# Optimization experiments

Hardware: AMD Instinct MI355X
Metric: run time of the kernel (lower is better)

The kernel has to match this reference:

```python
import jax, jax.numpy as jnp
import numpy as np

D_MODEL = 1024
D_STATE = 128
D_CONV = 4
EXPAND = 2
HEADDIM = 64
D_INNER = EXPAND * D_MODEL            # 2048
NHEADS = D_INNER // HEADDIM           # 32
D_IN_PROJ = 2 * D_INNER + 2 * D_STATE + NHEADS  # z, xBC, dt
CONV_DIM = D_INNER + 2 * D_STATE      # depthwise-conv channels


def setup_inputs() -> dict:
    key = jax.random.key(0)
    ks = jax.random.split(key, 8)
    B, L = 2, 2048
    s = lambda k, shape, sc=0.02: jax.random.normal(k, shape, jnp.float32) * sc
    return dict(
        x=jax.random.normal(ks[0], (B, L, D_MODEL), jnp.float32),
        norm1_w=jnp.ones((D_MODEL,), jnp.float32),
        in_proj_w=s(ks[1], (D_IN_PROJ, D_MODEL)),
        conv_w=s(ks[2], (CONV_DIM, D_CONV), 0.2),
        conv_b=jnp.zeros((CONV_DIM,), jnp.float32),
        dt_bias=jnp.log(jnp.expm1(jax.random.uniform(ks[3], (NHEADS,), jnp.float32, 0.001, 0.1))),
        A_log=jnp.log(jax.random.uniform(ks[4], (NHEADS,), jnp.float32, 1.0, 16.0)),
        D=jnp.ones((NHEADS,), jnp.float32),
        mnorm_w=jnp.ones((D_INNER,), jnp.float32),
        out_proj_w=s(ks[5], (D_MODEL, D_INNER)),
        norm2_w=jnp.ones((D_MODEL,), jnp.float32),
        mlp_w1=s(ks[6], (4 * D_MODEL, D_MODEL)),
        mlp_b1=jnp.zeros((4 * D_MODEL,), jnp.float32),
        mlp_w2=s(ks[7], (D_MODEL, 4 * D_MODEL)),
        mlp_b2=jnp.zeros((D_MODEL,), jnp.float32),
    )


def _block_norm(x, w, eps=1e-6):
    # Faithful to source: rms = sqrt(||x||_2^2 + eps) (their .mean(-1) is over a size-1 dim)
    return w * x / jnp.sqrt(jnp.sum(x * x, axis=-1, keepdims=True) + eps)


def _mamba2(x, in_proj_w, conv_w, conv_b, dt_bias, A_log, D, mnorm_w, out_proj_w):
    b, l, _ = x.shape
    zxbcdt = x @ in_proj_w.T                                   # (b,l,D_IN_PROJ)
    z, xBC, dt_raw = jnp.split(zxbcdt, [D_INNER, D_INNER + CONV_DIM], axis=-1)
    # causal depthwise conv1d + silu over (x,B,C)
    pad = jnp.pad(xBC, ((0, 0), (D_CONV - 1, 0), (0, 0)))
    conv = sum(pad[:, k:k + l, :] * conv_w[None, None, :, k] for k in range(D_CONV)) + conv_b
    xBC = jax.nn.silu(conv)
    xh, Bm, Cm = jnp.split(xBC, [D_INNER, D_INNER + D_STATE], axis=-1)
    xh = xh.reshape(b, l, NHEADS, HEADDIM)
    dt = jax.nn.softplus(dt_raw + dt_bias)                     # (b,l,h)
    A = -jnp.exp(A_log)                                        # (h,) scalar-A per head

    def step(hs, inp):
        x_t, dt_t, B_t, C_t = inp                              # (b,h,p),(b,h),(b,n),(b,n)
        dA = jnp.exp(dt_t * A)[:, :, None, None]               # (b,h,1,1)
        hs = hs * dA + (dt_t[:, :, None] * x_t)[..., None] * B_t[:, None, None, :]
        y_t = jnp.einsum('bhpn,bn->bhp', hs, C_t)
        return hs, y_t

    hs0 = jnp.zeros((b, NHEADS, HEADDIM, D_STATE), x.dtype)
    _, ys = jax.lax.scan(step, hs0, (xh.transpose(1, 0, 2, 3), dt.transpose(1, 0, 2),
                                     Bm.transpose(1, 0, 2), Cm.transpose(1, 0, 2)))
    y = ys.transpose(1, 0, 2, 3) + D[None, None, :, None] * xh  # D skip
    y = y.reshape(b, l, D_INNER)
    y = y * jax.nn.silu(z)                                      # gated RMSNorm (mamba2 default)
    y = y / jnp.sqrt(jnp.mean(y * y, axis=-1, keepdims=True) + 1e-5) * mnorm_w
    return y @ out_proj_w.T


def reference(x, norm1_w, in_proj_w, conv_w, conv_b, dt_bias, A_log, D, mnorm_w,
              out_proj_w, norm2_w, mlp_w1, mlp_b1, mlp_w2, mlp_b2):
    x = x + _mamba2(_block_norm(x, norm1_w), in_proj_w, conv_w, conv_b,
                    dt_bias, A_log, D, mnorm_w, out_proj_w)
    h = _block_norm(x, norm2_w)
    h = jax.nn.gelu(h @ mlp_w1.T + mlp_b1, approximate=False) @ mlp_w2.T + mlp_b2
    return x + h
```

## Files before the change

### kernel.cpp

```cpp
#include <hip/hip_runtime.h>
#include <hip/hip_bf16.h>
#include <cstdint>

#define L_SEQ   2048
#define BATCH   2
#define ROWS    (BATCH*L_SEQ)
#define DMODEL  1024
#define DINNER  2048
#define DSTATE  128
#define NHEADS  32
#define DIN_PROJ 4384
#define DIN_PAD  4480
#define CONVDIM  2304
#define DMLP    4096
#define CHUNK   64
#define NCHUNK  (L_SEQ/CHUNK)

typedef __attribute__((ext_vector_type(4))) float f32x4;
typedef __attribute__((ext_vector_type(8))) short bf16x8;
typedef __attribute__((ext_vector_type(4))) short bf16x4;
typedef __attribute__((ext_vector_type(2))) short bf16x2;

static __device__ __forceinline__ short f2bf(float f) {
  union { float f; unsigned int i; } v; v.f = f;
  unsigned int r = v.i + 0x7fffu + ((v.i >> 16) & 1u);
  return (short)(r >> 16);
}
static __device__ __forceinline__ float bf2f(short s) {
  union { unsigned int i; float f; } v; v.i = ((unsigned int)(unsigned short)s) << 16;
  return v.f;
}

static __device__ __forceinline__ void gl2lds16(const void* g, void* l) {
  __builtin_amdgcn_global_load_lds((const __attribute__((address_space(1))) void*)g,
                                   (__attribute__((address_space(3))) void*)l, 16, 0, 0);
}

__global__ __launch_bounds__(256) void cvt_kernel(const float* __restrict__ src, short* __restrict__ dst,
                                                  long rows_src, int kshift)
{
  long i = (((long)blockIdx.x) * 256 + threadIdx.x) * 4;
  long r = i >> kshift;
  bf16x4 o;
  if (r < rows_src) {
    f32x4 v = *(const f32x4*)&src[i];
    o[0] = f2bf(v[0]); o[1] = f2bf(v[1]); o[2] = f2bf(v[2]); o[3] = f2bf(v[3]);
  } else {
    o[0] = 0; o[1] = 0; o[2] = 0; o[3] = 0;
  }
  *(bf16x4*)&dst[i] = o;
}

__global__ __launch_bounds__(256) void rmsnorm_l2_kernel(const float* __restrict__ in,
                                                         const float* __restrict__ w,
                                                         short* __restrict__ out)
{
  int row = blockIdx.x, tid = threadIdx.x;
  const float* xr = in + (long)row * DMODEL;
  f32x4 v = *(const f32x4*)&xr[tid * 4];
  float s = v[0]*v[0] + v[1]*v[1] + v[2]*v[2] + v[3]*v[3];
  for (int o = 32; o; o >>= 1) s += __shfl_down(s, o);
  __shared__ float red[4];
  if ((tid & 63) == 0) red[tid >> 6] = s;
  __syncthreads();
  float sc = rsqrtf(red[0] + red[1] + red[2] + red[3] + 1e-6f);
  f32x4 wv = *(const f32x4*)&w[tid * 4];
  bf16x4 o;
  #pragma unroll
  for (int j = 0; j < 4; j++) o[j] = f2bf(v[j] * sc * wv[j]);
  *(bf16x4*)&out[(long)row * DMODEL + tid * 4] = o;
}

template<int EPI, int STG>
__global__ __launch_bounds__(256)
void gemm_bt_kernel(const short* __restrict__ A, const short* __restrict__ W,
                    const float* __restrict__ bias, const float* __restrict__ resid,
                    void* __restrict__ out, int N, int K)
{
  __shared__ short As[STG][128*64];
  __shared__ short Ws[STG][128*64];
  const int tid = threadIdx.x;
  const int lane = tid & 63, wid = tid >> 6;
  const int wm = wid >> 1, wn = wid & 1;
  const long arow0 = (long)blockIdx.x * 128;
  const long wrow0 = (long)blockIdx.y * 128;
  const int srow = tid >> 3;
  const int sslot = (tid & 7) ^ (srow & 7);
  const int sdst = (tid >> 3) * 64 + (tid & 7) * 8;

  f32x4 acc[4][4];
  #pragma unroll
  for (int m = 0; m < 4; m++)
    #pragma unroll
    for (int n = 0; n < 4; n++)
      #pragma unroll
      for (int j = 0; j < 4; j++) acc[m][n][j] = 0.f;

  auto stage = [&](int buf, int kt) {
    #pragma unroll
    for (int i = 0; i < 4; i++)
      gl2lds16(A + (arow0 + i*32 + srow) * (long)K + kt + sslot*8, &As[buf][i*2048 + sdst]);
    #pragma unroll
    for (int i = 0; i < 4; i++)
      gl2lds16(W + (wrow0 + i*32 + srow) * (long)K + kt + sslot*8, &Ws[buf][i*2048 + sdst]);
  };

  const int nt = K >> 6;
  #pragma unroll
  for (int s = 0; s < STG - 1; s++) stage(s, s << 6);

  const int swz = (lane & 7) << 3;
  for (int t = 0; t < nt; t++) {
    if (t + STG - 1 < nt) {
      stage((t + STG - 1) & (STG - 1), (t + STG - 1) << 6);
      if (STG == 4) asm volatile("s_waitcnt vmcnt(24)" ::: "memory");
      else          asm volatile("s_waitcnt vmcnt(8)"  ::: "memory");
    } else if (STG == 4 && t + 2 < nt) {
      asm volatile("s_waitcnt vmcnt(16)" ::: "memory");
    } else if (STG == 4 && t + 1 < nt) {
      asm volatile("s_waitcnt vmcnt(8)" ::: "memory");
    } else {
      asm volatile("s_waitcnt vmcnt(0)" ::: "memory");
    }
    __builtin_amdgcn_s_barrier();
    __builtin_amdgcn_sched_barrier(0);
    const int cur = t & (STG - 1);
    #pragma unroll
    for (int kk = 0; kk < 64; kk += 32) {
      bf16x8 a[4], b[4];
      const int ko = kk + (lane >> 4) * 8;
      #pragma unroll
      for (int m = 0; m < 4; m++) {
        int row = wm*64 + m*16 + (lane & 15);
        a[m] = *(const bf16x8*)&As[cur][(row*64 + ko) ^ swz];
      }
      #pragma unroll
      for (int n = 0; n < 4; n++) {
        int row = wn*64 + n*16 + (lane & 15);
        b[n] = *(const bf16x8*)&Ws[cur][(row*64 + ko) ^ swz];
      }
      #pragma unroll
      for (int m = 0; m < 4; m++)
        #pragma unroll
        for (int n = 0; n < 4; n++)
          acc[m][n] = __builtin_amdgcn_mfma_f32_16x16x32_bf16(a[m], b[n], acc[m][n], 0, 0, 0);
    }
    asm volatile("s_waitcnt lgkmcnt(0)" ::: "memory");
    __builtin_amdgcn_sched_barrier(0);
    __builtin_amdgcn_s_barrier();
  }

  const int colf = lane & 15, rowf = (lane >> 4) * 4;
  #pragma unroll
  for (int m = 0; m < 4; m++)
    #pragma unroll
    for (int n = 0; n < 4; n++) {
      long col = wrow0 + wn*64 + n*16 + colf;
      #pragma unroll
      for (int j = 0; j < 4; j++) {
        long row = arow0 + wm*64 + m*16 + rowf + j;
        long idx = row * (long)N + col;
        float v = acc[m][n][j];
        if (EPI == 0) {
          ((short*)out)[idx] = f2bf(v);
        } else if (EPI == 1) {
          ((float*)out)[idx] = v + resid[idx];
        } else if (EPI == 2) {
          float t = v + bias[col];
          float ge = 0.5f * t * (1.f + erff(t * 0.70710678118654752f));
          ((short*)out)[idx] = f2bf(ge);
        } else {
          ((float*)out)[idx] = v + bias[col] + resid[idx];
        }
      }
    }
}

__global__ __launch_bounds__(256) void conv_dt_kernel(
    const short* __restrict__ zx, const float* __restrict__ cw, const float* __restrict__ cb,
    const float* __restrict__ dt_bias,
    short* __restrict__ xh, short* __restrict__ Bo, short* __restrict__ Co, float* __restrict__ dto)
{
  const int r0 = blockIdx.x * 8;
  const int tid = threadIdx.x;
  const bool interior = (r0 & (L_SEQ - 1)) != 0;

  auto conv8 = [&](int c0, auto&& emit) {
    const long col = DINNER + c0;
    f32x4 w[8]; float cbv[8];
    #pragma unroll
    for (int j = 0; j < 8; j++) { w[j] = *(const f32x4*)&cw[(c0 + j) * 4]; cbv[j] = cb[c0 + j]; }
    bf16x8 win[11];
    #pragma unroll
    for (int j = 0; j < 3; j++) {
      bf16x8 z;
      #pragma unroll
      for (int q = 0; q < 8; q++) z[q] = 0;
      win[j] = interior ? *(const bf16x8*)&zx[(long)(r0 - 3 + j) * DIN_PAD + col] : z;
    }
    #pragma unroll
    for (int j = 3; j < 11; j++)
      win[j] = *(const bf16x8*)&zx[(long)(r0 - 3 + j) * DIN_PAD + col];
    #pragma unroll
    for (int i = 0; i < 8; i++) {
      float a[8];
      #pragma unroll
      for (int j = 0; j < 8; j++) a[j] = cbv[j];
      #pragma unroll
      for (int k = 0; k < 4; k++)
        #pragma unroll
        for (int j = 0; j < 8; j++) a[j] = fmaf(bf2f(win[i + k][j]), w[j][k], a[j]);
      bf16x8 o;
      #pragma unroll
      for (int j = 0; j < 8; j++) { float s = a[j] / (1.f + __expf(-a[j])); o[j] = f2bf(s); }
      emit(i, o);
    }
  };

  {
    int c0 = tid * 8;
    conv8(c0, [&](int i, bf16x8 o) {
      *(bf16x8*)&xh[(long)(r0 + i) * DINNER + c0] = o;
    });
  }
  if (tid < 32) {
    int c0 = 2048 + tid * 8;
    conv8(c0, [&](int i, bf16x8 o) {
      if (c0 < 2048 + DSTATE) *(bf16x8*)&Bo[(long)(r0 + i) * DSTATE + (c0 - 2048)] = o;
      else                    *(bf16x8*)&Co[(long)(r0 + i) * DSTATE + (c0 - 2048 - DSTATE)] = o;
    });
  } else if (tid < 36) {
    int h0 = (tid - 32) * 8;
    float db[8];
    #pragma unroll
    for (int j = 0; j < 8; j++) db[j] = dt_bias[h0 + j];
    #pragma unroll
    for (int i = 0; i < 8; i++) {
      bf16x8 v = *(const bf16x8*)&zx[(long)(r0 + i) * DIN_PAD + (DINNER + CONVDIM) + h0];
      f32x4 o0, o1;
      #pragma unroll
      for (int j = 0; j < 8; j++) {
        float t = bf2f(v[j]) + db[j];
        float sp = (t > 20.f) ? t : log1pf(__expf(t));
        if (j < 4) o0[j] = sp; else o1[j - 4] = sp;
      }
      *(f32x4*)&dto[(long)(r0 + i) * NHEADS + h0] = o0;
      *(f32x4*)&dto[(long)(r0 + i) * NHEADS + h0 + 4] = o1;
    }
  }
}


__global__ __launch_bounds__(256) void ssd_states_kernel(
    const short* __restrict__ xh, const short* __restrict__ Bm,
    const float* __restrict__ dtb, const float* __restrict__ A_log,
    float* __restrict__ CS, short* __restrict__ SC)
{
  int bid = blockIdx.x;
  int c = bid & 31, h = (bid >> 5) & 31, b = bid >> 10;
  long r0 = (long)b * L_SEQ + c * CHUNK;
  __shared__ short XT[64*72];
  __shared__ short BwT[128*72];
  __shared__ float ws[64];
  int tid = threadIdx.x;

  if (tid < 64) {
    float dtv = dtb[(r0 + tid)*NHEADS + h];
    float A = -__expf(A_log[h]);
    float v = dtv * A;
    #pragma unroll
    for (int o = 1; o < 64; o <<= 1) { float u = __shfl_up(v, o); if (tid >= o) v += u; }
    CS[(long)bid * 64 + tid] = v;
    float cs63 = __shfl(v, 63);
    ws[tid] = __expf(cs63 - v) * dtv;
  }
  #pragma unroll
  for (int i = 0; i < 2; i++) {
    int e = tid + i*256, tau = e & 63, p0 = (e >> 6) * 8;
    bf16x8 v = *(const bf16x8*)&xh[(r0 + tau)*DINNER + h*64 + p0];
    #pragma unroll
    for (int j = 0; j < 8; j++) XT[(p0 + j)*72 + tau] = v[j];
  }
  __syncthreads();
  #pragma unroll
  for (int i = 0; i < 4; i++) {
    int e = tid + i*256, tau = e & 63, n0 = (e >> 6) * 8;
    float w = ws[tau];
    bf16x8 v = *(const bf16x8*)&Bm[(r0 + tau)*DSTATE + n0];
    #pragma unroll
    for (int j = 0; j < 8; j++) BwT[(n0 + j)*72 + tau] = f2bf(bf2f(v[j]) * w);
  }
  __syncthreads();

  int lane = tid & 63, w = tid >> 6;
  f32x4 acc[8];
  #pragma unroll
  for (int nt = 0; nt < 8; nt++) { acc[nt][0]=0.f; acc[nt][1]=0.f; acc[nt][2]=0.f; acc[nt][3]=0.f; }
  #pragma unroll
  for (int kk = 0; kk < 64; kk += 32) {
    int ko = kk + (lane >> 4) * 8;
    bf16x8 a = *(const bf16x8*)&XT[(w*16 + (lane & 15))*72 + ko];
    #pragma unroll
    for (int nt = 0; nt < 8; nt++) {
      bf16x8 bfr = *(const bf16x8*)&BwT[(nt*16 + (lane & 15))*72 + ko];
      acc[nt] = __builtin_amdgcn_mfma_f32_16x16x32_bf16(a, bfr, acc[nt], 0, 0, 0);
    }
  }
  int colf = lane & 15, rowf = (lane >> 4) * 4;
  long sbase = (long)bid * 8192;
  #pragma unroll
  for (int nt = 0; nt < 8; nt++)
    #pragma unroll
    for (int j = 0; j < 4; j++)
      SC[sbase + (w*16 + rowf + j)*128 + nt*16 + colf] = f2bf(acc[nt][j]);
}

__global__ __launch_bounds__(256) void ssd_prefix_kernel(
    const short* __restrict__ SC, const float* __restrict__ CS, short* __restrict__ HP)
{
  int bid = blockIdx.x;
  int q = bid & 3, bh = bid >> 2;
  int tid = threadIdx.x;
  int p = q*16 + (tid >> 4);
  int n0 = (tid & 15) * 8;
  long base = (long)bh * NCHUNK * 8192 + (long)p*128 + n0;
  float H[8];
  #pragma unroll
  for (int j = 0; j < 8; j++) H[j] = 0.f;
  for (int c = 0; c < NCHUNK; c++) {
    long idx = base + (long)c * 8192;
    bf16x8 sc = *(const bf16x8*)&SC[idx];
    bf16x8 hv;
    #pragma unroll
    for (int j = 0; j < 8; j++) hv[j] = f2bf(H[j]);
    *(bf16x8*)&HP[idx] = hv;
    float r = __expf(CS[((long)bh * NCHUNK + c)*64 + 63]);
    #pragma unroll
    for (int j = 0; j < 8; j++) H[j] = H[j]*r + bf2f(sc[j]);
  }
}

__global__ __launch_bounds__(256) void ssd_out_kernel(
    const short* __restrict__ xh, const short* __restrict__ Bm, const short* __restrict__ Cm,
    const float* __restrict__ dtb, const float* __restrict__ CS,
    const short* __restrict__ HP, const float* __restrict__ Dvec,
    short* __restrict__ y)
{
  int bid = blockIdx.x;
  int c = bid & 31, h = (bid >> 5) & 31, b = bid >> 10;
  long r0 = (long)b * L_SEQ + c * CHUNK;
  __shared__ short Csh[64*136];
  __shared__ short Bsh[64*136];
  __shared__ short Ms[64*72];
  __shared__ short XT[64*72];
  __shared__ float csd[64], dts[64];
  int tid = threadIdx.x;

  if (tid < 64) {
    csd[tid] = CS[(long)bid*64 + tid];
    dts[tid] = dtb[(r0 + tid)*NHEADS + h];
  }
  #pragma unroll
  for (int i = 0; i < 4; i++) {
    int e = tid + i*256, tau = e >> 4, n0 = (e & 15) * 8;
    *(bf16x8*)&Bsh[tau*136 + n0] = *(const bf16x8*)&Bm[(r0 + tau)*DSTATE + n0];
    *(bf16x8*)&Csh[tau*136 + n0] = *(const bf16x8*)&Cm[(r0 + tau)*DSTATE + n0];
  }
  #pragma unroll
  for (int i = 0; i < 2; i++) {
    int e = tid + i*256, tau = e & 63, p0 = (e >> 6) * 8;
    bf16x8 v = *(const bf16x8*)&xh[(r0 + tau)*DINNER + h*64 + p0];
    #pragma unroll
    for (int j = 0; j < 8; j++) XT[(p0 + j)*72 + tau] = v[j];
  }
  __syncthreads();

  int lane = tid & 63, w = tid >> 6;
  int colf = lane & 15, rowf = (lane >> 4) * 4;

  f32x4 g[4];
  #pragma unroll
  for (int tt = 0; tt < 4; tt++) { g[tt][0]=0.f; g[tt][1]=0.f; g[tt][2]=0.f; g[tt][3]=0.f; }
  #pragma unroll
  for (int kk = 0; kk < 128; kk += 32) {
    int ko = kk + (lane >> 4) * 8;
    bf16x8 a = *(const bf16x8*)&Csh[(w*16 + (lane & 15))*136 + ko];
    #pragma unroll
    for (int tt = 0; tt < 4; tt++) {
      bf16x8 bfr = *(const bf16x8*)&Bsh[(tt*16 + (lane & 15))*136 + ko];
      g[tt] = __builtin_amdgcn_mfma_f32_16x16x32_bf16(a, bfr, g[tt], 0, 0, 0);
    }
  }
  #pragma unroll
  for (int tt = 0; tt < 4; tt++)
    #pragma unroll
    for (int j = 0; j < 4; j++) {
      int trow = w*16 + rowf + j;
      int tcol = tt*16 + colf;
      float m = (tcol <= trow) ? __expf(csd[trow] - csd[tcol]) * dts[tcol] * g[tt][j] : 0.f;
      Ms[trow*72 + tcol] = f2bf(m);
    }
  __syncthreads();

  f32x4 yv[4], yi[4];
  #pragma unroll
  for (int pt = 0; pt < 4; pt++) {
    yv[pt][0]=0.f; yv[pt][1]=0.f; yv[pt][2]=0.f; yv[pt][3]=0.f;
    yi[pt][0]=0.f; yi[pt][1]=0.f; yi[pt][2]=0.f; yi[pt][3]=0.f;
  }
  #pragma unroll
  for (int kk = 0; kk < 64; kk += 32) {
    int ko = kk + (lane >> 4) * 8;
    bf16x8 a = *(const bf16x8*)&Ms[(w*16 + (lane & 15))*72 + ko];
    #pragma unroll
    for (int pt = 0; pt < 4; pt++) {
      bf16x8 bfr = *(const bf16x8*)&XT[(pt*16 + (lane & 15))*72 + ko];
      yv[pt] = __builtin_amdgcn_mfma_f32_16x16x32_bf16(a, bfr, yv[pt], 0, 0, 0);
    }
  }
  long hpb = (long)bid * 8192;
  #pragma unroll
  for (int kk = 0; kk < 128; kk += 32) {
    int ko = kk + (lane >> 4) * 8;
    bf16x8 a = *(const bf16x8*)&Csh[(w*16 + (lane & 15))*136 + ko];
    #pragma unroll
    for (int pt = 0; pt < 4; pt++) {
      bf16x8 bfr = *(const bf16x8*)&HP[hpb + (long)(pt*16 + (lane & 15))*128 + ko];
      yi[pt] = __builtin_amdgcn_mfma_f32_16x16x32_bf16(a, bfr, yi[pt], 0, 0, 0);
    }
  }
  float Dh = Dvec[h];
  #pragma unroll
  for (int pt = 0; pt < 4; pt++)
    #pragma unroll
    for (int j = 0; j < 4; j++) {
      int trow = w*16 + rowf + j;
      int pcol = pt*16 + colf;
      float sc_ = __expf(csd[trow]);
      float xv = bf2f(XT[pcol*72 + trow]);
      y[(r0 + trow)*DINNER + h*64 + pcol] = f2bf(yv[pt][j] + sc_*yi[pt][j] + Dh*xv);
    }
}

__global__ __launch_bounds__(256) void gate_mnorm_kernel(
    const short* __restrict__ y, const short* __restrict__ zx, const float* __restrict__ mw,
    short* __restrict__ out)
{
  int row = blockIdx.x, tid = threadIdx.x;
  int c0 = tid * 8;
  bf16x8 yv = *(const bf16x8*)&y[(long)row*DINNER + c0];
  bf16x8 zv = *(const bf16x8*)&zx[(long)row*DIN_PAD + c0];
  float g[8]; float ssum = 0.f;
  #pragma unroll
  for (int j = 0; j < 8; j++) {
    float z = bf2f(zv[j]);
    float v = bf2f(yv[j]) * (z / (1.f + __expf(-z)));
    g[j] = v; ssum += v * v;
  }
  for (int o = 32; o; o >>= 1) ssum += __shfl_down(ssum, o);
  __shared__ float red[4];
  if ((tid & 63) == 0) red[tid >> 6] = ssum;
  __syncthreads();
  float tot = red[0] + red[1] + red[2] + red[3];
  float sc = rsqrtf(tot * (1.0f / DINNER) + 1e-5f);
  bf16x8 o;
  #pragma unroll
  for (int j = 0; j < 8; j++) o[j] = f2bf(g[j] * sc * mw[c0 + j]);
  *(bf16x8*)&out[(long)row*DINNER + c0] = o;
}

extern "C" void kernel_launch(void* const* d_in, const int* in_sizes, int n_in,
                              void* d_out, int out_size, void* d_ws, size_t ws_size,
                              hipStream_t stream)
{
  const float* x        = (const float*)d_in[0];
  const float* norm1_w  = (const float*)d_in[1];
  const float* in_proj  = (const float*)d_in[2];
  const float* conv_w   = (const float*)d_in[3];
  const float* conv_b   = (const float*)d_in[4];
  const float* dt_bias  = (const float*)d_in[5];
  const float* A_log    = (const float*)d_in[6];
  const float* Dvec     = (const float*)d_in[7];
  const float* mnorm_w  = (const float*)d_in[8];
  const float* out_proj = (const float*)d_in[9];
  const float* norm2_w  = (const float*)d_in[10];
  const float* mlp_w1   = (const float*)d_in[11];
  const float* mlp_b1   = (const float*)d_in[12];
  const float* mlp_w2   = (const float*)d_in[13];
  const float* mlp_b2   = (const float*)d_in[14];
  float* outp = (float*)d_out;

  uint8_t* wsp = (uint8_t*)d_ws;
  auto take = [&](size_t bytes) { void* p = wsp; wsp += (bytes + 255) & ~(size_t)255; return p; };
  short* W1B  = (short*)take((size_t)DIN_PAD * DMODEL * 2);
  short* W2B  = (short*)take((size_t)DMODEL * DINNER * 2);
  short* W3B  = (short*)take((size_t)DMLP * DMODEL * 2);
  short* W4B  = (short*)take((size_t)DMODEL * DMLP * 2);
  short* X1B  = (short*)take((size_t)ROWS * DMODEL * 2);
  short* ZX   = (short*)take((size_t)ROWS * DIN_PAD * 2);
  short* XH   = (short*)take((size_t)ROWS * DINNER * 2);
  short* BMb  = (short*)take((size_t)ROWS * DSTATE * 2);
  short* CMb  = (short*)take((size_t)ROWS * DSTATE * 2);
  float* DTb  = (float*)take((size_t)ROWS * NHEADS * 4);
  short* Yb   = (short*)take((size_t)ROWS * DINNER * 2);
  short* YGB  = (short*)take((size_t)ROWS * DINNER * 2);
  float* X2   = (float*)take((size_t)ROWS * DMODEL * 4);
  short* X2NB = (short*)take((size_t)ROWS * DMODEL * 2);
  short* H1B  = (short*)take((size_t)ROWS * DMLP * 2);

  short* SC = H1B;
  short* HP = YGB;
  float* CS = (float*)X2NB;

  cvt_kernel<<<4480, 256, 0, stream>>>(in_proj, W1B, DIN_PROJ, 10);
  cvt_kernel<<<2048, 256, 0, stream>>>(out_proj, W2B, DMODEL, 11);
  cvt_kernel<<<4096, 256, 0, stream>>>(mlp_w1, W3B, DMLP, 10);
  cvt_kernel<<<4096, 256, 0, stream>>>(mlp_w2, W4B, DMODEL, 12);

  rmsnorm_l2_kernel<<<ROWS, 256, 0, stream>>>(x, norm1_w, X1B);
  gemm_bt_kernel<0,2><<<dim3(ROWS/128, DIN_PAD/128), 256, 0, stream>>>(X1B, W1B, nullptr, nullptr, ZX, DIN_PAD, DMODEL);
  conv_dt_kernel<<<ROWS/8, 256, 0, stream>>>(ZX, conv_w, conv_b, dt_bias, XH, BMb, CMb, DTb);
  ssd_states_kernel<<<BATCH*NHEADS*NCHUNK, 256, 0, stream>>>(XH, BMb, DTb, A_log, CS, SC);
  ssd_prefix_kernel<<<BATCH*NHEADS*4, 256, 0, stream>>>(SC, CS, HP);
  ssd_out_kernel<<<BATCH*NHEADS*NCHUNK, 256, 0, stream>>>(XH, BMb, CMb, DTb, CS, HP, Dvec, Yb);
  gate_mnorm_kernel<<<ROWS, 256, 0, stream>>>(Yb, ZX, mnorm_w, YGB);
  gemm_bt_kernel<1,4><<<dim3(ROWS/128, DMODEL/128), 256, 0, stream>>>(YGB, W2B, nullptr, x, X2, DMODEL, DINNER);
  rmsnorm_l2_kernel<<<ROWS, 256, 0, stream>>>(X2, norm2_w, X2NB);
  gemm_bt_kernel<2,2><<<dim3(ROWS/128, DMLP/128), 256, 0, stream>>>(X2NB, W3B, mlp_b1, nullptr, H1B, DMLP, DMODEL);
  gemm_bt_kernel<3,4><<<dim3(ROWS/128, DMODEL/128), 256, 0, stream>>>(H1B, W4B, mlp_b2, X2, outp, DMODEL, DMLP);
}
```

Baseline: 355.3 us.

## Split-K the two N=1024 GEMMs with a separate reduction kernel

```diff
diff --git a/kernel.cpp b/kernel.cpp
--- a/kernel.cpp
+++ b/kernel.cpp
@@ -88,6 +88,9 @@
   const int sslot = (tid & 7) ^ (srow & 7);
   const int sdst = (tid >> 3) * 64 + (tid & 7) * 8;
 
+  const int Keff = K / gridDim.z;
+  const long kbase = (long)blockIdx.z * Keff;
+
   f32x4 acc[4][4];
   #pragma unroll
   for (int m = 0; m < 4; m++)
@@ -96,7 +99,7 @@
       #pragma unroll
       for (int j = 0; j < 4; j++) acc[m][n][j] = 0.f;
 
-  auto stage = [&](int buf, int kt) {
+  auto stage = [&](int buf, long kt) {
     #pragma unroll
     for (int i = 0; i < 4; i++)
       gl2lds16(A + (arow0 + i*32 + srow) * (long)K + kt + sslot*8, &As[buf][i*2048 + sdst]);
@@ -105,14 +108,14 @@
       gl2lds16(W + (wrow0 + i*32 + srow) * (long)K + kt + sslot*8, &Ws[buf][i*2048 + sdst]);
   };
 
-  const int nt = K >> 6;
-  #pragma unroll
-  for (int s = 0; s < STG - 1; s++) stage(s, s << 6);
+  const int nt = Keff >> 6;
+  #pragma unroll
+  for (int s = 0; s < STG - 1; s++) stage(s, kbase + (s << 6));
 
   const int swz = (lane & 7) << 3;
   for (int t = 0; t < nt; t++) {
     if (t + STG - 1 < nt) {
-      stage((t + STG - 1) & (STG - 1), (t + STG - 1) << 6);
+      stage((t + STG - 1) & (STG - 1), kbase + ((long)(t + STG - 1) << 6));
       if (STG == 4) asm volatile("s_waitcnt vmcnt(24)" ::: "memory");
       else          asm volatile("s_waitcnt vmcnt(8)"  ::: "memory");
     } else if (STG == 4 && t + 2 < nt) {
@@ -151,6 +154,7 @@
   }
 
   const int colf = lane & 15, rowf = (lane >> 4) * 4;
+  const long psliceoff = (long)blockIdx.z * ((long)gridDim.x * 128) * N;
   #pragma unroll
   for (int m = 0; m < 4; m++)
     #pragma unroll
@@ -163,17 +167,36 @@
         float v = acc[m][n][j];
         if (EPI == 0) {
           ((short*)out)[idx] = f2bf(v);
-        } else if (EPI == 1) {
-          ((float*)out)[idx] = v + resid[idx];
         } else if (EPI == 2) {
           float t = v + bias[col];
           float ge = 0.5f * t * (1.f + erff(t * 0.70710678118654752f));
           ((short*)out)[idx] = f2bf(ge);
         } else {
-          ((float*)out)[idx] = v + bias[col] + resid[idx];
+          ((float*)out)[psliceoff + idx] = v;
         }
       }
     }
+}
+
+template<bool BIAS>
+__global__ __launch_bounds__(256) void reduce_split2_kernel(
+    const float* __restrict__ part, const float* __restrict__ resid,
+    const float* __restrict__ bias, float* __restrict__ out)
+{
+  long i = ((long)blockIdx.x * 256 + threadIdx.x) * 4;
+  f32x4 p0 = *(const f32x4*)&part[i];
+  f32x4 p1 = *(const f32x4*)&part[i + (long)ROWS * DMODEL];
+  f32x4 r  = *(const f32x4*)&resid[i];
+  f32x4 o;
+  if (BIAS) {
+    f32x4 bv = *(const f32x4*)&bias[(int)(i & (DMODEL - 1))];
+    #pragma unroll
+    for (int j = 0; j < 4; j++) o[j] = p0[j] + p1[j] + r[j] + bv[j];
+  } else {
+    #pragma unroll
+    for (int j = 0; j < 4; j++) o[j] = p0[j] + p1[j] + r[j];
+  }
+  *(f32x4*)&out[i] = o;
 }
 
 __global__ __launch_bounds__(256) void conv_dt_kernel(
@@ -511,6 +534,7 @@
   short* SC = H1B;
   short* HP = YGB;
   float* CS = (float*)X2NB;
+  float* PART = (float*)ZX;
 
   cvt_kernel<<<4480, 256, 0, stream>>>(in_proj, W1B, DIN_PROJ, 10);
   cvt_kernel<<<2048, 256, 0, stream>>>(out_proj, W2B, DMODEL, 11);
@@ -524,8 +548,10 @@
   ssd_prefix_kernel<<<BATCH*NHEADS*4, 256, 0, stream>>>(SC, CS, HP);
   ssd_out_kernel<<<BATCH*NHEADS*NCHUNK, 256, 0, stream>>>(XH, BMb, CMb, DTb, CS, HP, Dvec, Yb);
   gate_mnorm_kernel<<<ROWS, 256, 0, stream>>>(Yb, ZX, mnorm_w, YGB);
-  gemm_bt_kernel<1,4><<<dim3(ROWS/128, DMODEL/128), 256, 0, stream>>>(YGB, W2B, nullptr, x, X2, DMODEL, DINNER);
+  gemm_bt_kernel<4,2><<<dim3(ROWS/128, DMODEL/128, 2), 256, 0, stream>>>(YGB, W2B, nullptr, nullptr, PART, DMODEL, DINNER);
+  reduce_split2_kernel<false><<<ROWS*DMODEL/1024, 256, 0, stream>>>(PART, x, nullptr, X2);
   rmsnorm_l2_kernel<<<ROWS, 256, 0, stream>>>(X2, norm2_w, X2NB);
   gemm_bt_kernel<2,2><<<dim3(ROWS/128, DMLP/128), 256, 0, stream>>>(X2NB, W3B, mlp_b1, nullptr, H1B, DMLP, DMODEL);
-  gemm_bt_kernel<3,4><<<dim3(ROWS/128, DMODEL/128), 256, 0, stream>>>(H1B, W4B, mlp_b2, X2, outp, DMODEL, DMLP);
-}
+  gemm_bt_kernel<4,2><<<dim3(ROWS/128, DMODEL/128, 2), 256, 0, stream>>>(H1B, W4B, nullptr, nullptr, PART, DMODEL, DMLP);
+  reduce_split2_kernel<true><<<ROWS*DMODEL/1024, 256, 0, stream>>>(PART, X2, mlp_b2, outp);
+}
```

Result: faster. 337.6 us (-5.0%).

## Add 256x256 GEMM kernel with split-K for out_proj and MLP GEMMs

Applied to the files above, without the earlier changes.

```diff
diff --git a/kernel.cpp b/kernel.cpp
--- a/kernel.cpp
+++ b/kernel.cpp
@@ -96,7 +96,7 @@
       #pragma unroll
       for (int j = 0; j < 4; j++) acc[m][n][j] = 0.f;
 
-  auto stage = [&](int buf, int kt) {
+  auto stage = [&](int buf, long kt) {
     #pragma unroll
     for (int i = 0; i < 4; i++)
       gl2lds16(A + (arow0 + i*32 + srow) * (long)K + kt + sslot*8, &As[buf][i*2048 + sdst]);
@@ -112,13 +112,8 @@
   const int swz = (lane & 7) << 3;
   for (int t = 0; t < nt; t++) {
     if (t + STG - 1 < nt) {
-      stage((t + STG - 1) & (STG - 1), (t + STG - 1) << 6);
-      if (STG == 4) asm volatile("s_waitcnt vmcnt(24)" ::: "memory");
-      else          asm volatile("s_waitcnt vmcnt(8)"  ::: "memory");
-    } else if (STG == 4 && t + 2 < nt) {
-      asm volatile("s_waitcnt vmcnt(16)" ::: "memory");
-    } else if (STG == 4 && t + 1 < nt) {
-      asm volatile("s_waitcnt vmcnt(8)" ::: "memory");
+      stage((t + STG - 1) & (STG - 1), (long)(t + STG - 1) << 6);
+      asm volatile("s_waitcnt vmcnt(8)"  ::: "memory");
     } else {
       asm volatile("s_waitcnt vmcnt(0)" ::: "memory");
     }
@@ -160,20 +155,151 @@
       for (int j = 0; j < 4; j++) {
         long row = arow0 + wm*64 + m*16 + rowf + j;
         long idx = row * (long)N + col;
+        ((short*)out)[idx] = f2bf(acc[m][n][j]);
+      }
+    }
+}
+
+template<int EPI>
+__global__ __launch_bounds__(512)
+void gemm256_kernel(const short* __restrict__ A, const short* __restrict__ W,
+                    const float* __restrict__ bias, void* __restrict__ out, int N, int K)
+{
+  __shared__ short As[2][2][8192];
+  __shared__ short Bs[2][2][8192];
+  const int tid = threadIdx.x;
+  const int lane = tid & 63, wid = tid >> 6;
+  const int wm = wid >> 2, wn = wid & 3;
+  const long arow0 = (long)blockIdx.x * 256;
+  const long wrow0 = (long)blockIdx.y * 256;
+  const int Kslice = K / gridDim.z;
+  const long kbase = (long)blockIdx.z * Kslice;
+  const int ntiles = Kslice >> 6;
+
+  const int sr0 = tid >> 2, sr1 = sr0 + 128;
+  const int ss  = tid & 3;
+  const int scb0 = ss ^ ((sr0 >> 1) & 3);
+  const int scb1 = ss ^ ((sr1 >> 1) & 3);
+  const int sdst0 = tid * 8, sdst1 = tid * 8 + 4096;
+
+  auto stageA = [&](int tau, int kh) {
+    long colb = kbase + (long)tau * 64 + kh * 32;
+    gl2lds16(A + (arow0 + sr0) * (long)K + colb + scb0 * 8, &As[tau & 1][kh][sdst0]);
+    gl2lds16(A + (arow0 + sr1) * (long)K + colb + scb1 * 8, &As[tau & 1][kh][sdst1]);
+  };
+  auto stageB = [&](int tau, int kh) {
+    long colb = kbase + (long)tau * 64 + kh * 32;
+    gl2lds16(W + (wrow0 + sr0) * (long)K + colb + scb0 * 8, &Bs[tau & 1][kh][sdst0]);
+    gl2lds16(W + (wrow0 + sr1) * (long)K + colb + scb1 * 8, &Bs[tau & 1][kh][sdst1]);
+  };
+
+  f32x4 acc[8][4];
+  #pragma unroll
+  for (int m = 0; m < 8; m++)
+    #pragma unroll
+    for (int n = 0; n < 4; n++)
+      #pragma unroll
+      for (int j = 0; j < 4; j++) acc[m][n][j] = 0.f;
+
+  const int li = lane & 15;
+  const int rcb = (((lane >> 4) ^ ((li >> 1) & 3))) * 8;
+
+  stageA(0,0); stageB(0,0); stageA(0,1); stageB(0,1); stageA(1,0); stageB(1,0);
+  asm volatile("s_waitcnt vmcnt(8)" ::: "memory");
+  __builtin_amdgcn_s_barrier();
+
+  bf16x8 a[8];
+  auto phase = [&](int g, int kh, int nh) {
+    const int buf = g & 1;
+    if (nh == 0) {
+      #pragma unroll
+      for (int m = 0; m < 8; m++)
+        a[m] = *(const bf16x8*)&As[buf][kh][(wm*128 + m*16 + li)*32 + rcb];
+    }
+    bf16x8 b0 = *(const bf16x8*)&Bs[buf][kh][(wn*64 + (nh*2    )*16 + li)*32 + rcb];
+    bf16x8 b1 = *(const bf16x8*)&Bs[buf][kh][(wn*64 + (nh*2 + 1)*16 + li)*32 + rcb];
+    if (kh == 0) {
+      if (g + 1 < ntiles) { if (nh == 0) stageA(g+1, 1); else stageB(g+1, 1); }
+    } else {
+      if (g + 2 < ntiles) { if (nh == 0) stageA(g+2, 0); else stageB(g+2, 0); }
+    }
+    __builtin_amdgcn_s_barrier();
+    asm volatile("s_waitcnt lgkmcnt(0)" ::: "memory");
+    __builtin_amdgcn_sched_barrier(0);
+    __builtin_amdgcn_s_setprio(1);
+    #pragma unroll
+    for (int m = 0; m < 8; m++) {
+      acc[m][nh*2    ] = __builtin_amdgcn_mfma_f32_16x16x32_bf16(a[m], b0, acc[m][nh*2    ], 0, 0, 0);
+      acc[m][nh*2 + 1] = __builtin_amdgcn_mfma_f32_16x16x32_bf16(a[m], b1, acc[m][nh*2 + 1], 0, 0, 0);
+    }
+    __builtin_amdgcn_s_setprio(0);
+    if (kh == 0 && nh == 1) {
+      if (g < ntiles - 1) asm volatile("s_waitcnt vmcnt(8)" ::: "memory");
+      else                asm volatile("s_waitcnt vmcnt(0)" ::: "memory");
+    } else if (kh == 1 && nh == 1 && g < ntiles - 1) {
+      if (g < ntiles - 2) asm volatile("s_waitcnt vmcnt(8)" ::: "memory");
+      else                asm volatile("s_waitcnt vmcnt(4)" ::: "memory");
+    }
+    __builtin_amdgcn_s_barrier();
+  };
+
+  for (int g = 0; g < ntiles; ++g) {
+    phase(g, 0, 0); phase(g, 0, 1); phase(g, 1, 0); phase(g, 1, 1);
+  }
+
+  const int colf = lane & 15, rowf = (lane >> 4) * 4;
+  const long MN = (long)gridDim.x * 256 * N;
+  const long po = (long)blockIdx.z * MN;
+  #pragma unroll
+  for (int m = 0; m < 8; m++)
+    #pragma unroll
+    for (int n = 0; n < 4; n++) {
+      long col = wrow0 + wn*64 + n*16 + colf;
+      #pragma unroll
+      for (int j = 0; j < 4; j++) {
+        long row = arow0 + wm*128 + m*16 + rowf + j;
+        long idx = row * (long)N + col;
         float v = acc[m][n][j];
-        if (EPI == 0) {
-          ((short*)out)[idx] = f2bf(v);
-        } else if (EPI == 1) {
-          ((float*)out)[idx] = v + resid[idx];
-        } else if (EPI == 2) {
+        if (EPI == 2) {
           float t = v + bias[col];
           float ge = 0.5f * t * (1.f + erff(t * 0.70710678118654752f));
           ((short*)out)[idx] = f2bf(ge);
         } else {
-          ((float*)out)[idx] = v + bias[col] + resid[idx];
+          ((short*)out)[po + idx] = f2bf(v);
         }
       }
     }
+}
+
+template<bool BIAS>
+__global__ __launch_bounds__(256) void reduce_split4_kernel(
+    const short* __restrict__ part, const float* __restrict__ resid,
+    const float* __restrict__ bias, float* __restrict__ out)
+{
+  long i = ((long)blockIdx.x * 256 + threadIdx.x) * 8;
+  const long MN = (long)ROWS * DMODEL;
+  bf16x8 p0 = *(const bf16x8*)&part[i];
+  bf16x8 p1 = *(const bf16x8*)&part[i + MN];
+  bf16x8 p2 = *(const bf16x8*)&part[i + 2*MN];
+  bf16x8 p3 = *(const bf16x8*)&part[i + 3*MN];
+  f32x4 r0 = *(const f32x4*)&resid[i];
+  f32x4 r1 = *(const f32x4*)&resid[i + 4];
+  f32x4 o0, o1;
+  #pragma unroll
+  for (int j = 0; j < 8; j++) {
+    float s = (bf2f(p0[j]) + bf2f(p1[j])) + (bf2f(p2[j]) + bf2f(p3[j]));
+    s += (j < 4) ? r0[j] : r1[j - 4];
+    if (j < 4) o0[j] = s; else o1[j - 4] = s;
+  }
+  if (BIAS) {
+    int c = (int)(i & (DMODEL - 1));
+    f32x4 b0 = *(const f32x4*)&bias[c];
+    f32x4 b1 = *(const f32x4*)&bias[c + 4];
+    #pragma unroll
+    for (int j = 0; j < 4; j++) { o0[j] += b0[j]; o1[j] += b1[j]; }
+  }
+  *(f32x4*)&out[i] = o0;
+  *(f32x4*)&out[i + 4] = o1;
 }
 
 __global__ __launch_bounds__(256) void conv_dt_kernel(
@@ -511,6 +637,7 @@
   short* SC = H1B;
   short* HP = YGB;
   float* CS = (float*)X2NB;
+  short* PART = ZX;
 
   cvt_kernel<<<4480, 256, 0, stream>>>(in_proj, W1B, DIN_PROJ, 10);
   cvt_kernel<<<2048, 256, 0, stream>>>(out_proj, W2B, DMODEL, 11);
@@ -524,8 +651,10 @@
   ssd_prefix_kernel<<<BATCH*NHEADS*4, 256, 0, stream>>>(SC, CS, HP);
   ssd_out_kernel<<<BATCH*NHEADS*NCHUNK, 256, 0, stream>>>(XH, BMb, CMb, DTb, CS, HP, Dvec, Yb);
   gate_mnorm_kernel<<<ROWS, 256, 0, stream>>>(Yb, ZX, mnorm_w, YGB);
-  gemm_bt_kernel<1,4><<<dim3(ROWS/128, DMODEL/128), 256, 0, stream>>>(YGB, W2B, nullptr, x, X2, DMODEL, DINNER);
+  gemm256_kernel<4><<<dim3(16, 4, 4), 512, 0, stream>>>(YGB, W2B, nullptr, PART, DMODEL, DINNER);
+  reduce_split4_kernel<false><<<2048, 256, 0, stream>>>(PART, x, nullptr, X2);
   rmsnorm_l2_kernel<<<ROWS, 256, 0, stream>>>(X2, norm2_w, X2NB);
-  gemm_bt_kernel<2,2><<<dim3(ROWS/128, DMLP/128), 256, 0, stream>>>(X2NB, W3B, mlp_b1, nullptr, H1B, DMLP, DMODEL);
-  gemm_bt_kernel<3,4><<<dim3(ROWS/128, DMODEL/128), 256, 0, stream>>>(H1B, W4B, mlp_b2, X2, outp, DMODEL, DMLP);
-}
+  gemm256_kernel<2><<<dim3(16, 16, 1), 512, 0, stream>>>(X2NB, W3B, mlp_b1, H1B, DMLP, DMODEL);
+  gemm256_kernel<4><<<dim3(16, 4, 4), 512, 0, stream>>>(H1B, W4B, nullptr, PART, DMODEL, DMLP);
+  reduce_split4_kernel<true><<<2048, 256, 0, stream>>>(PART, X2, mlp_b2, outp);
+}
```

New measurement: 338.4 us. 1.05x faster.
